# Optimization experiments

Measured on AMD Instinct MI355X. Metric: run time of the kernel, lower is better.

## Reference

```python
import jax, jax.numpy as jnp
import numpy as np

B, L, N = 32, 512, 512          # batch, seq_len, enc_in (num variables = token dim)
D, H, EL, DF = 512, 8, 2, 2048  # d_model, n_heads (hardcoded 8 in FourierBlock), e_layers, d_ff
PRED, K, MODES = 96, 25, 64     # pred_len, moving_avg kernel, fourier modes (low select)
E = D // H


def setup_inputs() -> dict:
    key = jax.random.key(0)
    ks = jax.random.split(key, 16)
    s = 0.02
    return {
        "x_enc": jax.random.normal(ks[0], (B, L, N), jnp.float32),
        "x_mark_enc": jax.random.normal(ks[1], (B, L, 4), jnp.float32),
        "x_dec": jax.random.normal(ks[2], (B, 144, N), jnp.float32),
        "x_mark_dec": jax.random.normal(ks[3], (B, 144, 4), jnp.float32),
        "W_trend": jax.random.normal(ks[4], (L, PRED), jnp.float32) * s,
        "b_trend": jnp.zeros((PRED,), jnp.float32),
        "W_emb": jax.random.normal(ks[5], (L, D), jnp.float32) * s,
        "b_emb": jnp.zeros((D,), jnp.float32),
        "Wq": jax.random.normal(ks[6], (EL, D, D), jnp.float32) * s,
        "bq": jnp.zeros((EL, D), jnp.float32),
        "Wk": jax.random.normal(ks[7], (EL, D, D), jnp.float32) * s,
        "bk": jnp.zeros((EL, D), jnp.float32),
        "Wv": jax.random.normal(ks[8], (EL, D, D), jnp.float32) * s,
        "bv": jnp.zeros((EL, D), jnp.float32),
        "fw_r": jax.random.uniform(ks[9], (EL, H, E, E, MODES), jnp.float32) / (D * D),
        "fw_i": jax.random.uniform(ks[10], (EL, H, E, E, MODES), jnp.float32) / (D * D),
        "Wo": jax.random.normal(ks[11], (EL, D, D), jnp.float32) * s,
        "bo": jnp.zeros((EL, D), jnp.float32),
        "W1": jax.random.normal(ks[12], (EL, DF, D), jnp.float32) * s,
        "W2": jax.random.normal(ks[13], (EL, D, DF), jnp.float32) * s,
        "ln_g": jnp.ones((D,), jnp.float32),
        "ln_b": jnp.zeros((D,), jnp.float32),
        "W_head": jax.random.normal(ks[14], (D, PRED), jnp.float32) * s,
        "b_head": jnp.zeros((PRED,), jnp.float32),
    }


def series_decomp(x, k):
    # moving average over axis=1 with edge replication padding (Autoformer style)
    pad = (k - 1) // 2
    xp = jnp.concatenate([jnp.repeat(x[:, :1], pad, axis=1), x,
                          jnp.repeat(x[:, -1:], pad, axis=1)], axis=1)
    c = jnp.cumsum(xp, axis=1)
    c = jnp.concatenate([jnp.zeros_like(c[:, :1]), c], axis=1)
    mean = (c[:, k:] - c[:, :-k]) / k
    return x - mean, mean


def fourier_attn(x, Wq, bq, Wk, bk, Wv, bv, fw, Wo, bo):
    # AutoCorrelationLayer wrapping FourierBlock (k/v projections computed but unused)
    b, n, d = x.shape
    q = (x @ Wq + bq).reshape(b, n, H, E)
    _k = (x @ Wk + bk).reshape(b, n, H, E)
    _v = (x @ Wv + bv).reshape(b, n, H, E)
    xq = jnp.transpose(q, (0, 2, 3, 1))        # [B,H,E,N]
    x_ft = jnp.fft.rfft(xq, axis=-1)           # [B,H,E,N//2+1]
    m = fw.shape[-1]
    # low-frequency mode select: index = range(m); out_ft[..., wi] = einsum('bhi,hio->bho')
    out_sel = jnp.einsum('bhim,hiom->bhom', x_ft[..., :m], fw)
    out_ft = jnp.zeros((b, H, E, n // 2 + 1), x_ft.dtype).at[..., :m].set(out_sel)
    xt = jnp.fft.irfft(out_ft, n=n, axis=-1)   # [B,H,E,N]
    out = xt.reshape(b, n, H * E)              # replicates torch .view(B, L, -1) on [B,H,E,L]
    return out @ Wo + bo


def encoder_layer(x, Wq, bq, Wk, bk, Wv, bv, fw, Wo, bo, W1, W2):
    x = x + fourier_attn(x, Wq, bq, Wk, bk, Wv, bv, fw, Wo, bo)
    x, _ = series_decomp(x, K)
    y = jax.nn.gelu(x @ W1.T, approximate=False) @ W2.T  # 1x1 convs, bias=False
    x, _ = series_decomp(x + y, K)
    return x


def my_layernorm(x, g, b):
    mu = jnp.mean(x, -1, keepdims=True)
    var = jnp.var(x, -1, keepdims=True)
    xh = (x - mu) / jnp.sqrt(var + 1e-5) * g + b
    return xh - jnp.mean(xh, axis=1, keepdims=True)  # my_Layernorm: subtract seq-mean


def reference(x_enc, x_mark_enc, x_dec, x_mark_dec, W_trend, b_trend, W_emb, b_emb,
              Wq, bq, Wk, bk, Wv, bv, fw_r, fw_i, Wo, bo, W1, W2, ln_g, ln_b,
              W_head, b_head):
    seasonal, trend = series_decomp(x_enc, K)                         # [B,L,N]
    trend_out = jnp.einsum('bln,lp->bpn', trend, W_trend) + b_trend[None, :, None]
    enc = jnp.einsum('bln,ld->bnd', seasonal, W_emb) + b_emb          # variate tokens [B,N,D]
    for i in range(EL):
        fw = fw_r[i] + 1j * fw_i[i]
        enc = encoder_layer(enc, Wq[i], bq[i], Wk[i], bk[i], Wv[i], bv[i],
                            fw, Wo[i], bo[i], W1[i], W2[i])
    enc = my_layernorm(enc, ln_g, ln_b)
    seasonal_out = jnp.transpose(enc @ W_head + b_head, (0, 2, 1))    # [B,pred,N]
    return seasonal_out + trend_out
```

## Files before the change

### kernel.cpp

```cpp
#include <hip/hip_runtime.h>
#include <math.h>


typedef unsigned short ushort_t;
typedef unsigned int uint_t;
using bf16x8_t = __attribute__((ext_vector_type(8))) short;
using f32x4_t  = __attribute__((ext_vector_type(4))) float;
using u16x8_t  = __attribute__((ext_vector_type(8))) unsigned short;

__device__ __forceinline__ unsigned short f2b(float x) {
    union { float f; uint_t u; } c; c.f = x;
    uint_t r = c.u + 0x7fffu + ((c.u >> 16) & 1u);
    return (unsigned short)(r >> 16);
}
__device__ __forceinline__ float b2f(unsigned short h) {
    union { uint_t u; float f; } c; c.u = ((uint_t)h) << 16; return c.f;
}
__device__ __forceinline__ float gelu_fast(float x) {
    float z = x * (1.5957691216f + 0.0713548163f * x * x);
    return x / (1.f + __expf(-z));
}

#define GCAST(p) ((const __attribute__((address_space(1))) void*)(p))
#define LCAST(p) ((__attribute__((address_space(3))) void*)(p))

enum { ME_F32 = 0, ME_BF16, ME_DCBIAS_BF16, ME_BIASCOL_BF16,
       ME_BIASCOL_ACCB16, ME_GELU_BF16, ME_RESB_BF16, ME_TREND };

template<int EPI>
__global__ __launch_bounds__(512)
void mgemm_k(const ushort_t* __restrict__ A, const ushort_t* __restrict__ B,
             const float* __restrict__ bias, const ushort_t* __restrict__ Resb,
             void* __restrict__ Cv,
             int M, int N, int K, int ldc, int ldres,
             long sA, long sB, long sC, long sRes)
{
    const int gx = gridDim.x, gy = gridDim.y;
    const int nwg = gx * gy * gridDim.z;
    const int lin = (blockIdx.z * gy + blockIdx.y) * gx + blockIdx.x;
    const int cpx = nwg >> 3;
    const int swz = (nwg & 7) ? lin : ((lin & 7) * cpx + (lin >> 3));
    const int bx = swz % gx;
    const int t2 = swz / gx;
    const int by = t2 % gy;
    const int bz = t2 / gy;

    A += bz * sA;
    B += bz * sB;
    const int m0 = by * 128, n0 = bx * 128;

    __shared__ __align__(16) ushort_t As[3][4096];
    __shared__ __align__(16) ushort_t Bs[3][4096];

    const int tid = threadIdx.x;
    const int wave = tid >> 6, lane = tid & 63;
    const int wr = wave >> 1, wc = wave & 1;

    f32x4_t acc[2][4] = {};

    const int srow = tid >> 2;
    const int skof = (((tid & 3) ^ ((tid >> 2) & 3)) << 3);

    const ushort_t* ga = A + (long)(m0 + srow) * K + skof;
    const ushort_t* gb = B + (long)(n0 + srow) * K + skof;
    const int nt = K >> 5;

#define STG(s, bidx) { const long ko = (long)(s) << 5; \
    __builtin_amdgcn_global_load_lds(GCAST(ga + ko), LCAST(As[bidx] + wave * 512), 16, 0, 0); \
    __builtin_amdgcn_global_load_lds(GCAST(gb + ko), LCAST(Bs[bidx] + wave * 512), 16, 0, 0); }

    STG(0, 0)
    STG(1, 1)

    const int q = lane >> 4;
    int cbuf = 0;

    for (int t = 0; t < nt; ++t) {
        if (t + 1 < nt) { asm volatile("s_waitcnt vmcnt(2)" ::: "memory"); }
        else            { asm volatile("s_waitcnt vmcnt(0)" ::: "memory"); }
        __builtin_amdgcn_s_barrier();
        asm volatile("" ::: "memory");
        __builtin_amdgcn_sched_barrier(0);
        if (t + 2 < nt) { int nb = cbuf + 2; if (nb >= 3) nb -= 3; STG(t + 2, nb) }

        bf16x8_t a[2], b[4];
        #pragma unroll
        for (int i = 0; i < 2; ++i) {
            int ra = wr * 32 + i * 16 + (lane & 15);
            a[i] = *(const bf16x8_t*)&As[cbuf][ra * 32 + ((q ^ (ra & 3)) << 3)];
        }
        #pragma unroll
        for (int j = 0; j < 4; ++j) {
            int rb = wc * 64 + j * 16 + (lane & 15);
            b[j] = *(const bf16x8_t*)&Bs[cbuf][rb * 32 + ((q ^ (rb & 3)) << 3)];
        }
        #pragma unroll
        for (int i = 0; i < 2; ++i)
            #pragma unroll
            for (int j = 0; j < 4; ++j)
                acc[i][j] = __builtin_amdgcn_mfma_f32_16x16x32_bf16(a[i], b[j], acc[i][j], 0, 0, 0);
        ++cbuf; if (cbuf >= 3) cbuf = 0;
    }
#undef STG

    float*    Cf  = (float*)Cv + bz * sC;
    ushort_t* Cb  = (ushort_t*)Cv + bz * sC;
    const ushort_t* R = Resb ? Resb + bz * sRes : nullptr;

    #pragma unroll
    for (int i = 0; i < 2; ++i) {
        #pragma unroll
        for (int j = 0; j < 4; ++j) {
            #pragma unroll
            for (int r = 0; r < 4; ++r) {
                int gm = m0 + wr * 32 + i * 16 + (lane >> 4) * 4 + r;
                int gn = n0 + wc * 64 + j * 16 + (lane & 15);
                float v = acc[i][j][r];
                long idx = (long)gm * ldc + gn;
                if (EPI == ME_F32)               Cf[idx] = v;
                else if (EPI == ME_BF16)         Cb[idx] = f2b(v);
                else if (EPI == ME_BIASCOL_BF16) Cb[idx] = f2b(v + bias[gn]);
                else if (EPI == ME_BIASCOL_ACCB16) Cb[idx] = f2b(b2f(Cb[idx]) + v + bias[gn]);
                else if (EPI == ME_GELU_BF16)    Cb[idx] = f2b(gelu_fast(v));
                else if (EPI == ME_RESB_BF16)    Cb[idx] = f2b(v + b2f(R[(long)gm * ldres + gn]));
            }
        }
    }
}

template<int EPI>
__global__ __launch_bounds__(256)
void sgemm_k(const ushort_t* __restrict__ A, const ushort_t* __restrict__ B,
             const float* __restrict__ bias, void* __restrict__ Cv,
             int M, int N, int K, int ldc,
             long sA, long sB, long sC)
{
    const int gx = gridDim.x, gy = gridDim.y;
    const int nwg = gx * gy * gridDim.z;
    const int lin = (blockIdx.z * gy + blockIdx.y) * gx + blockIdx.x;
    const int cpx = nwg >> 3;
    const int swz = (nwg & 7) ? lin : ((lin & 7) * cpx + (lin >> 3));
    const int bx = swz % gx;
    const int t2 = swz / gx;
    const int by = t2 % gy;
    const int bz = t2 / gy;

    A += bz * sA;
    B += bz * sB;
    const int m0 = by * 64, n0 = bx * 64;

    __shared__ __align__(16) ushort_t As[3][2048];
    __shared__ __align__(16) ushort_t Bs[3][2048];

    const int tid = threadIdx.x;
    const int wave = tid >> 6, lane = tid & 63;
    const int wr = wave >> 1, wc = wave & 1;

    f32x4_t acc[2][2] = {};

    const int srow = tid >> 2;
    const int skof = (((tid & 3) ^ ((tid >> 2) & 3)) << 3);

    const ushort_t* ga = A + (long)(m0 + srow) * K + skof;
    const ushort_t* gb = B + (long)(n0 + srow) * K + skof;
    const int nt = K >> 5;

#define STG(s, bidx) { const long ko = (long)(s) << 5; \
    __builtin_amdgcn_global_load_lds(GCAST(ga + ko), LCAST(As[bidx] + wave * 512), 16, 0, 0); \
    __builtin_amdgcn_global_load_lds(GCAST(gb + ko), LCAST(Bs[bidx] + wave * 512), 16, 0, 0); }

    STG(0, 0)
    STG(1, 1)

    const int q = lane >> 4;
    int cbuf = 0;

    for (int t = 0; t < nt; ++t) {
        if (t + 1 < nt) { asm volatile("s_waitcnt vmcnt(2)" ::: "memory"); }
        else            { asm volatile("s_waitcnt vmcnt(0)" ::: "memory"); }
        __builtin_amdgcn_s_barrier();
        asm volatile("" ::: "memory");
        __builtin_amdgcn_sched_barrier(0);
        if (t + 2 < nt) { int nb = cbuf + 2; if (nb >= 3) nb -= 3; STG(t + 2, nb) }

        bf16x8_t a[2], b[2];
        #pragma unroll
        for (int i = 0; i < 2; ++i) {
            int ra = wr * 32 + i * 16 + (lane & 15);
            a[i] = *(const bf16x8_t*)&As[cbuf][ra * 32 + ((q ^ (ra & 3)) << 3)];
        }
        #pragma unroll
        for (int j = 0; j < 2; ++j) {
            int rb = wc * 32 + j * 16 + (lane & 15);
            b[j] = *(const bf16x8_t*)&Bs[cbuf][rb * 32 + ((q ^ (rb & 3)) << 3)];
        }
        #pragma unroll
        for (int i = 0; i < 2; ++i)
            #pragma unroll
            for (int j = 0; j < 2; ++j)
                acc[i][j] = __builtin_amdgcn_mfma_f32_16x16x32_bf16(a[i], b[j], acc[i][j], 0, 0, 0);
        ++cbuf; if (cbuf >= 3) cbuf = 0;
    }
#undef STG

    float*    Cf = (float*)Cv + bz * sC;
    ushort_t* Cb = (ushort_t*)Cv + bz * sC;

    #pragma unroll
    for (int i = 0; i < 2; ++i) {
        #pragma unroll
        for (int j = 0; j < 2; ++j) {
            #pragma unroll
            for (int r = 0; r < 4; ++r) {
                int gm = m0 + wr * 32 + i * 16 + (lane >> 4) * 4 + r;
                int gn = n0 + wc * 32 + j * 16 + (lane & 15);
                float v = acc[i][j][r];
                long idx = (long)gm * ldc + gn;
                if (EPI == ME_F32)               Cf[idx] = v;
                else if (EPI == ME_BF16)         Cb[idx] = f2b(v);
                else if (EPI == ME_DCBIAS_BF16)  Cb[idx] = f2b(v + (gn == 0 ? 512.f * bias[gm] : 0.f));
                else if (EPI == ME_TREND) { if (gm < 96) Cf[idx] = v + bias[gm]; }
            }
        }
    }
}

__global__ __launch_bounds__(256)
void fmix_k(const ushort_t* __restrict__ A2, const ushort_t* __restrict__ B2,
            ushort_t* __restrict__ OS)
{
    const int hm = blockIdx.x;
    const int h = hm >> 6, m = hm & 63;
    __shared__ __align__(16) ushort_t As[32 * 128];
    __shared__ __align__(16) ushort_t Bs[128 * 128];

    const int tid = threadIdx.x;
    const int w = tid >> 6, lane = tid & 63;

    const ushort_t* Ag = A2 + (long)hm * 4096;
    const ushort_t* Bg = B2 + (long)hm * 16384;
    #pragma unroll
    for (int r = 0; r < 2; ++r) {
        int rowA = w * 8 + r * 4 + (lane >> 4);
        const ushort_t* src = Ag + rowA * 128 + (((lane & 15) ^ (rowA & 15)) << 3);
        __builtin_amdgcn_global_load_lds(GCAST(src), LCAST(As + w * 1024 + r * 512), 16, 0, 0);
    }
    #pragma unroll
    for (int r = 0; r < 8; ++r) {
        int rowB = w * 32 + r * 4 + (lane >> 4);
        const ushort_t* src = Bg + rowB * 128 + (((lane & 15) ^ (rowB & 15)) << 3);
        __builtin_amdgcn_global_load_lds(GCAST(src), LCAST(Bs + w * 4096 + r * 512), 16, 0, 0);
    }
    __syncthreads();

    f32x4_t acc[2][2] = {};
    #pragma unroll
    for (int kk = 0; kk < 4; ++kk) {
        const int cq = kk * 4 + (lane >> 4);
        bf16x8_t a[2], b[2];
        #pragma unroll
        for (int i = 0; i < 2; ++i) {
            int ra = i * 16 + (lane & 15);
            a[i] = *(const bf16x8_t*)&As[ra * 128 + ((cq ^ (ra & 15)) << 3)];
        }
        #pragma unroll
        for (int j = 0; j < 2; ++j) {
            int rb = w * 32 + j * 16 + (lane & 15);
            b[j] = *(const bf16x8_t*)&Bs[rb * 128 + ((cq ^ (rb & 15)) << 3)];
        }
        #pragma unroll
        for (int i = 0; i < 2; ++i)
            #pragma unroll
            for (int j = 0; j < 2; ++j)
                acc[i][j] = __builtin_amdgcn_mfma_f32_16x16x32_bf16(a[i], b[j], acc[i][j], 0, 0, 0);
    }

    #pragma unroll
    for (int i = 0; i < 2; ++i) {
        #pragma unroll
        for (int j = 0; j < 2; ++j) {
            #pragma unroll
            for (int r = 0; r < 4; ++r) {
                int b = i * 16 + (lane >> 4) * 4 + r;
                int n2 = w * 32 + j * 16 + (lane & 15);
                int o = n2 & 63, ri = n2 >> 6;
                OS[((long)b * 512 + h * 64 + o) * 128 + ri * 64 + m] = f2b(acc[i][j][r]);
            }
        }
    }
}

__global__ __launch_bounds__(256)
void bprep_k(const float* __restrict__ FR, const float* __restrict__ FI,
             ushort_t* __restrict__ B2)
{
    const int bx = blockIdx.x;
    const int h = bx >> 6, o = bx & 63;
    __shared__ float fr_s[64][65];
    __shared__ float fi_s[64][65];
    for (int e = threadIdx.x; e < 4096; e += 256) {
        int i = e >> 6, m = e & 63;
        long src = ((long)(h * 64 + i) * 64 + o) * 64 + m;
        fr_s[i][m] = FR[src];
        fi_s[i][m] = FI[src];
    }
    __syncthreads();
    const int m = threadIdx.x & 63;
    const int kq = threadIdx.x >> 6;
    ushort_t* b0 = B2 + ((long)(h * 64 + m) * 128 + o) * 128;
    ushort_t* b1 = B2 + ((long)(h * 64 + m) * 128 + o + 64) * 128;
    for (int kk = 0; kk < 32; ++kk) {
        int k2 = kq * 32 + kk;
        int ik = k2 & 63, hi = k2 >> 6;
        float fr = fr_s[ik][m], fi = fi_s[ik][m];
        b0[k2] = f2b(hi ? -fi : fr);
        b1[k2] = f2b(hi ?  fr : fi);
    }
}

__global__ __launch_bounds__(256)
void aprep_k(const ushort_t* __restrict__ XFTb, ushort_t* __restrict__ A2)
{
    const int bx = blockIdx.x;
    const int b = bx >> 3, h = bx & 7;
    __shared__ ushort_t xs[64][130];
    for (int e = threadIdx.x; e < 8192; e += 256) {
        int i = e >> 7, mp = e & 127;
        xs[i][mp] = XFTb[((long)b * 512 + h * 64 + i) * 128 + mp];
    }
    __syncthreads();
    const int m = threadIdx.x & 63;
    const int kq = threadIdx.x >> 6;
    ushort_t* dst = A2 + ((long)(h * 64 + m) * 32 + b) * 128;
    for (int kk = 0; kk < 32; ++kk) {
        int k2 = kq * 32 + kk;
        int i = k2 & 63, ri = k2 >> 6;
        dst[k2] = xs[i][ri * 64 + m];
    }
}

__global__ __launch_bounds__(256)
void decomp2t_k(const float* __restrict__ X, ushort_t* __restrict__ SbT,
                ushort_t* __restrict__ TrbT)
{
    const int id = blockIdx.x;
    const int ch = id & 1, rc = (id >> 1) & 31, b = id >> 6;
    const int c = ch * 256 + threadIdx.x;
    const int r0 = rc * 16;
    const long base = ((long)b << 18) + c;
    float s = 0.f;
    #pragma unroll
    for (int j = -12; j <= 12; ++j) {
        int rr = r0 + j; rr = rr < 0 ? 0 : (rr > 511 ? 511 : rr);
        s += X[base + ((long)rr << 9)];
    }
    u16x8_t sv0, sv1, tv0, tv1;
    for (int rr = 0; rr < 16; ++rr) {
        int r = r0 + rr;
        float mean = s * (1.f / 25.f);
        float x = X[base + ((long)r << 9)];
        if (rr < 8) { sv0[rr] = f2b(x - mean); tv0[rr] = f2b(mean); }
        else        { sv1[rr - 8] = f2b(x - mean); tv1[rr - 8] = f2b(mean); }
        int rp = r + 13; rp = rp > 511 ? 511 : rp;
        int rm = r - 12; rm = rm < 0 ? 0 : rm;
        s += X[base + ((long)rp << 9)] - X[base + ((long)rm << 9)];
    }
    long obase = (long)b * 262144 + (long)c * 512 + r0;
    *(u16x8_t*)&SbT[obase] = sv0;  *(u16x8_t*)&SbT[obase + 8] = sv1;
    *(u16x8_t*)&TrbT[obase] = tv0; *(u16x8_t*)&TrbT[obase + 8] = tv1;
}

__global__ __launch_bounds__(256)
void decomp2v_k(const ushort_t* __restrict__ Xb, ushort_t* __restrict__ Sb)
{
    const int id = blockIdx.x;
    const int b = id >> 4, rc = id & 15;
    const int c0 = (threadIdx.x & 63) * 8;
    const int rsub = threadIdx.x >> 6;
    const int r0 = rc * 32 + rsub * 8;
    const ushort_t* base = Xb + ((long)b << 18) + c0;
    ushort_t* obase = Sb + ((long)b << 18) + c0;

    float s[8] = {};
    #pragma unroll
    for (int j = -12; j <= 12; ++j) {
        int rr = r0 + j; rr = rr < 0 ? 0 : (rr > 511 ? 511 : rr);
        u16x8_t v = *(const u16x8_t*)(base + ((long)rr << 9));
        #pragma unroll
        for (int k = 0; k < 8; ++k) s[k] += b2f(v[k]);
    }
    for (int rr = 0; rr < 8; ++rr) {
        int r = r0 + rr;
        u16x8_t xv = *(const u16x8_t*)(base + ((long)r << 9));
        u16x8_t ov;
        #pragma unroll
        for (int k = 0; k < 8; ++k) ov[k] = f2b(b2f(xv[k]) - s[k] * (1.f / 25.f));
        *(u16x8_t*)(obase + ((long)r << 9)) = ov;
        int rp = r + 13; rp = rp > 511 ? 511 : rp;
        int rm = r - 12; rm = rm < 0 ? 0 : rm;
        u16x8_t vp = *(const u16x8_t*)(base + ((long)rp << 9));
        u16x8_t vm = *(const u16x8_t*)(base + ((long)rm << 9));
        #pragma unroll
        for (int k = 0; k < 8; ++k) s[k] += b2f(vp[k]) - b2f(vm[k]);
    }
}

__global__ __launch_bounds__(256)
void init_tables_k(ushort_t* __restrict__ TFb, ushort_t* __restrict__ TI2b)
{
    int t = blockIdx.x * 256 + threadIdx.x;
    const float w = 6.283185307179586f / 512.f;
    if (t < 65536) {
        int mp = t >> 9, n = t & 511;
        int m = mp & 63;
        float ang = ((m * n) & 511) * w;
        TFb[t] = f2b((mp < 64) ? cosf(ang) : -sinf(ang));
    } else {
        int u = t - 65536;
        int mp = u >> 9, n = u & 511;
        int m = mp & 63;
        float ang = ((m * n) & 511) * w;
        float v;
        if (mp < 64) v = (m == 0) ? (1.f / 512.f) : (2.f / 512.f) * cosf(ang);
        else         v = (m == 0) ? 0.f : -(2.f / 512.f) * sinf(ang);
        TI2b[u] = f2b(v);
    }
}

__global__ __launch_bounds__(256)
void f2b_k(const float* __restrict__ X, ushort_t* __restrict__ Y, long n)
{
    long i = ((long)blockIdx.x * 256 + threadIdx.x) * 8;
    if (i >= n) return;
    const float4* xp = (const float4*)(X + i);
    float4 v0 = xp[0], v1 = xp[1];
    u16x8_t o;
    o[0] = f2b(v0.x); o[1] = f2b(v0.y); o[2] = f2b(v0.z); o[3] = f2b(v0.w);
    o[4] = f2b(v1.x); o[5] = f2b(v1.y); o[6] = f2b(v1.z); o[7] = f2b(v1.w);
    *(u16x8_t*)(Y + i) = o;
}

__global__ __launch_bounds__(256)
void trans_b_k(const float* __restrict__ X, ushort_t* __restrict__ Y,
               int R, int C, long sX, long sY)
{
    __shared__ float t[32][33];
    X += (long)blockIdx.z * sX;
    Y += (long)blockIdx.z * sY;
    int r0 = blockIdx.y * 32, c0 = blockIdx.x * 32;
    int tx = threadIdx.x & 31, ty = threadIdx.x >> 5;
    #pragma unroll
    for (int i = ty; i < 32; i += 8)
        t[i][tx] = X[(long)(r0 + i) * C + c0 + tx];
    __syncthreads();
    #pragma unroll
    for (int i = ty; i < 32; i += 8)
        Y[(long)(c0 + i) * R + r0 + tx] = f2b(t[tx][i]);
}

__global__ __launch_bounds__(256)
void trans_bb_k(const ushort_t* __restrict__ X, ushort_t* __restrict__ Y,
                int R, int C, long sX, long sY)
{
    __shared__ ushort_t t[32][34];
    X += (long)blockIdx.z * sX;
    Y += (long)blockIdx.z * sY;
    int r0 = blockIdx.y * 32, c0 = blockIdx.x * 32;
    int tx = threadIdx.x & 31, ty = threadIdx.x >> 5;
    #pragma unroll
    for (int i = ty; i < 32; i += 8)
        t[i][tx] = X[(long)(r0 + i) * C + c0 + tx];
    __syncthreads();
    #pragma unroll
    for (int i = ty; i < 32; i += 8)
        Y[(long)(c0 + i) * R + r0 + tx] = t[tx][i];
}

__global__ __launch_bounds__(256)
void ln_rows_bb_k(const ushort_t* __restrict__ Xb, const float* __restrict__ g,
                  const float* __restrict__ bta, ushort_t* __restrict__ Yb)
{
    int wave = threadIdx.x >> 6, lane = threadIdx.x & 63;
    long row = (long)blockIdx.x * 4 + wave;
    const ushort_t* x = Xb + row * 512 + lane * 8;
    u16x8_t v = *(const u16x8_t*)x;
    float f[8];
    float s = 0.f, ss = 0.f;
    #pragma unroll
    for (int j = 0; j < 8; ++j) { f[j] = b2f(v[j]); s += f[j]; ss += f[j] * f[j]; }
    #pragma unroll
    for (int o = 32; o; o >>= 1) { s += __shfl_xor(s, o); ss += __shfl_xor(ss, o); }
    float mu = s * (1.f / 512.f);
    float var = ss * (1.f / 512.f) - mu * mu;
    float inv = rsqrtf(var + 1e-5f);
    u16x8_t ov;
    #pragma unroll
    for (int j = 0; j < 8; ++j)
        ov[j] = f2b((f[j] - mu) * inv * g[lane * 8 + j] + bta[lane * 8 + j]);
    *(u16x8_t*)(Yb + row * 512 + lane * 8) = ov;
}

__global__ __launch_bounds__(256)
void colmean_bb_k(const ushort_t* __restrict__ Y, ushort_t* __restrict__ O)
{
    __shared__ float ps[4][64];
    int b = blockIdx.x, dg = blockIdx.y;
    int wave = threadIdx.x >> 6, lane = threadIdx.x & 63;
    int d = dg * 64 + lane;
    long base = (long)b * 262144 + d;
    float s = 0.f;
    for (int t = wave * 128; t < wave * 128 + 128; ++t)
        s += b2f(Y[base + ((long)t << 9)]);
    ps[wave][lane] = s;
    __syncthreads();
    float mean = (ps[0][lane] + ps[1][lane] + ps[2][lane] + ps[3][lane]) * (1.f / 512.f);
    for (int t = wave * 128; t < wave * 128 + 128; ++t)
        O[base + ((long)t << 9)] = f2b(b2f(Y[base + ((long)t << 9)]) - mean);
}

__global__ __launch_bounds__(256)
void headadd_k(const float* __restrict__ Th, const float* __restrict__ bh,
               float* __restrict__ out)
{
    const int id = blockIdx.x;
    const int b = id >> 4, t0 = (id & 15) * 32;
    __shared__ float tile[32][100];
    for (int e = threadIdx.x; e < 32 * 96; e += 256) {
        int tl = e / 96, p = e - tl * 96;
        tile[tl][p] = Th[((long)(b * 512 + t0 + tl)) * 128 + p];
    }
    __syncthreads();
    for (int e = threadIdx.x; e < 96 * 32; e += 256) {
        int p = e >> 5, tl = e & 31;
        out[(long)b * 49152 + p * 512 + t0 + tl] += tile[tl][p] + bh[p];
    }
}

extern "C" void kernel_launch(void* const* d_in, const int* in_sizes, int n_in,
                              void* d_out, int out_size, void* d_ws, size_t ws_size,
                              hipStream_t stream)
{
    const float* x_enc   = (const float*)d_in[0];
    const float* W_trend = (const float*)d_in[4];
    const float* b_trend = (const float*)d_in[5];
    const float* W_emb   = (const float*)d_in[6];
    const float* b_emb   = (const float*)d_in[7];
    const float* Wq      = (const float*)d_in[8];
    const float* bq      = (const float*)d_in[9];
    const float* fw_r    = (const float*)d_in[14];
    const float* fw_i    = (const float*)d_in[15];
    const float* Wo      = (const float*)d_in[16];
    const float* bo      = (const float*)d_in[17];
    const float* W1      = (const float*)d_in[18];
    const float* W2      = (const float*)d_in[19];
    const float* ln_g    = (const float*)d_in[20];
    const float* ln_b    = (const float*)d_in[21];
    const float* W_head  = (const float*)d_in[22];
    const float* b_head  = (const float*)d_in[23];
    float* out = (float*)d_out;
    float* ws  = (float*)d_ws;

    const long F = 8388608;
    float* G    = ws;
    ushort_t* xw  = (ushort_t*)(ws + 3 * F);
    ushort_t* xs  = (ushort_t*)(ws + 4 * F);
    ushort_t* T1b = xs + 8388608;
    ushort_t* qT  = (ushort_t*)(ws + 5 * F);

    ushort_t* trendT = (ushort_t*)G;
    ushort_t* XFTb  = (ushort_t*)G;
    ushort_t* Yb    = (ushort_t*)(G + 1048576);
    ushort_t* A2    = (ushort_t*)(G + 2097152);
    ushort_t* OSELb = (ushort_t*)(G + 3145728);
    ushort_t* xbT   = (ushort_t*)(G + 4194304);
    ushort_t* B2    = (ushort_t*)(G + 8388608);
    float*    Thead = G;
    ushort_t* gb    = (ushort_t*)G;

    ushort_t* WembT  = (ushort_t*)(ws + 6 * F);
    ushort_t* WTq2   = WembT + 262144;
    ushort_t* WTo2   = WTq2 + 524288;
    ushort_t* W1b2   = WTo2 + 524288;
    ushort_t* W2b2   = W1b2 + 2097152;
    ushort_t* TFb    = W2b2 + 2097152;
    ushort_t* TI2b   = TFb + 65536;
    ushort_t* WtT    = TI2b + 65536;
    ushort_t* WheadT = WtT + 65536;
    ushort_t* TIWob2 = WheadT + 65536;

    dim3 blk(256), blk5(512);

    init_tables_k<<<dim3(512), blk, 0, stream>>>(TFb, TI2b);

    decomp2t_k<<<dim3(2048), blk, 0, stream>>>(x_enc, qT, trendT);

    trans_b_k<<<dim3(3, 16, 1), blk, 0, stream>>>(W_trend, WtT, 512, 96, 0L, 0L);
    trans_b_k<<<dim3(3, 16, 1), blk, 0, stream>>>(W_head, WheadT, 512, 96, 0L, 0L);
    trans_b_k<<<dim3(16, 16, 1), blk, 0, stream>>>(W_emb, WembT, 512, 512, 0L, 0L);
    trans_b_k<<<dim3(16, 16, 2), blk, 0, stream>>>(Wq, WTq2, 512, 512, 262144L, 262144L);
    trans_b_k<<<dim3(16, 16, 2), blk, 0, stream>>>(Wo, WTo2, 512, 512, 262144L, 262144L);
    f2b_k<<<dim3(1024), blk, 0, stream>>>(W1, W1b2, 2097152L);
    f2b_k<<<dim3(1024), blk, 0, stream>>>(W2, W2b2, 2097152L);
    sgemm_k<ME_BF16><<<dim3(2, 8, 2), blk, 0, stream>>>(
        WTo2, TI2b, nullptr, TIWob2,
        512, 128, 512, 128, 262144L, 0L, 65536L);

    sgemm_k<ME_TREND><<<dim3(8, 2, 32), blk, 0, stream>>>(
        WtT, trendT, b_trend, out,
        128, 512, 512, 512, 0L, 262144L, 49152L);

    mgemm_k<ME_BIASCOL_BF16><<<dim3(4, 4, 32), blk5, 0, stream>>>(
        qT, WembT, b_emb, nullptr, xw,
        512, 512, 512, 512, 0, 262144L, 0L, 262144L, 0L);

    for (int l = 0; l < 2; ++l) {
        const float* bq_l = bq + (long)l * 512;
        const float* bo_l = bo + (long)l * 512;
        const float* fr_l = fw_r + (long)l * 2097152;
        const float* fi_l = fw_i + (long)l * 2097152;
        const ushort_t* WTq_l   = WTq2 + (long)l * 262144;
        const ushort_t* W1b_l   = W1b2 + (long)l * 1048576;
        const ushort_t* W2b_l   = W2b2 + (long)l * 1048576;
        const ushort_t* TIWob_l = TIWob2 + (long)l * 65536;

        bprep_k<<<dim3(512), blk, 0, stream>>>(fr_l, fi_l, B2);

        trans_bb_k<<<dim3(16, 16, 32), blk, 0, stream>>>(xw, xbT, 512, 512, 262144L, 262144L);

        sgemm_k<ME_BF16><<<dim3(8, 2, 32), blk, 0, stream>>>(
            TFb, xbT, nullptr, Yb,
            128, 512, 512, 512, 0L, 262144L, 65536L);

        sgemm_k<ME_DCBIAS_BF16><<<dim3(2, 8, 32), blk, 0, stream>>>(
            WTq_l, Yb, bq_l, XFTb,
            512, 128, 512, 128, 0L, 65536L, 65536L);

        aprep_k<<<dim3(256), blk, 0, stream>>>(XFTb, A2);
        fmix_k<<<dim3(512), blk, 0, stream>>>(A2, B2, OSELb);

        mgemm_k<ME_BIASCOL_ACCB16><<<dim3(4, 128, 1), blk5, 0, stream>>>(
            OSELb, TIWob_l, bo_l, nullptr, xw,
            16384, 512, 128, 512, 0, 0L, 0L, 0L, 0L);

        decomp2v_k<<<dim3(512), blk, 0, stream>>>(xw, xs);

        mgemm_k<ME_GELU_BF16><<<dim3(16, 128, 1), blk5, 0, stream>>>(
            xs, W1b_l, nullptr, nullptr, gb,
            16384, 2048, 512, 2048, 0, 0L, 0L, 0L, 0L);
        mgemm_k<ME_RESB_BF16><<<dim3(4, 128, 1), blk5, 0, stream>>>(
            gb, W2b_l, nullptr, xs, T1b,
            16384, 512, 2048, 512, 512, 0L, 0L, 0L, 0L);

        decomp2v_k<<<dim3(512), blk, 0, stream>>>(T1b, xw);
    }

    ln_rows_bb_k<<<dim3(4096), blk, 0, stream>>>(xw, ln_g, ln_b, T1b);
    colmean_bb_k<<<dim3(32, 8), blk, 0, stream>>>(T1b, xs);

    sgemm_k<ME_F32><<<dim3(2, 256, 1), blk, 0, stream>>>(
        xs, WheadT, nullptr, Thead,
        16384, 128, 512, 128, 0L, 0L, 0L);

    headadd_k<<<dim3(512), blk, 0, stream>>>(Thead, b_head, out);
}
```

Before: 546.1 us.

## Halve mgemm block to four waves with larger per-wave tiles, drop LDS swizzle

The 128x128 mgemm now runs with 256 threads instead of 512. Each wave computes a 64x64 sub-tile (4x4 MFMA accumulators) instead of 32x64, and each thread issues two global-to-LDS loads per operand per stage. The XOR swizzle on the LDS layout is removed in favour of a plain row-major 32-wide layout. The aim is more MFMA work per LDS fragment load and fewer waves to synchronise, at the cost of more accumulator registers, lower occupancy, and likely LDS bank conflicts on the fragment reads.

```diff
diff --git a/kernel.cpp b/kernel.cpp
--- a/kernel.cpp
+++ b/kernel.cpp
@@ -28,7 +28,7 @@
        ME_BIASCOL_ACCB16, ME_GELU_BF16, ME_RESB_BF16, ME_TREND };
 
 template<int EPI>
-__global__ __launch_bounds__(512)
+__global__ __launch_bounds__(256)
 void mgemm_k(const ushort_t* __restrict__ A, const ushort_t* __restrict__ B,
              const float* __restrict__ bias, const ushort_t* __restrict__ Resb,
              void* __restrict__ Cv,
@@ -56,46 +56,42 @@
     const int wave = tid >> 6, lane = tid & 63;
     const int wr = wave >> 1, wc = wave & 1;
 
-    f32x4_t acc[2][4] = {};
-
-    const int srow = tid >> 2;
-    const int skof = (((tid & 3) ^ ((tid >> 2) & 3)) << 3);
-
-    const ushort_t* ga = A + (long)(m0 + srow) * K + skof;
-    const ushort_t* gb = B + (long)(n0 + srow) * K + skof;
+    f32x4_t acc[4][4] = {};
+
+    const ushort_t* ga = A + (long)(m0 + wave * 32 + (lane >> 2)) * K + (lane & 3) * 8;
+    const ushort_t* gb = B + (long)(n0 + wave * 32 + (lane >> 2)) * K + (lane & 3) * 8;
+    const long row16 = (long)16 * K;
     const int nt = K >> 5;
 
 #define STG(s, bidx) { const long ko = (long)(s) << 5; \
-    __builtin_amdgcn_global_load_lds(GCAST(ga + ko), LCAST(As[bidx] + wave * 512), 16, 0, 0); \
-    __builtin_amdgcn_global_load_lds(GCAST(gb + ko), LCAST(Bs[bidx] + wave * 512), 16, 0, 0); }
+    __builtin_amdgcn_global_load_lds(GCAST(ga + ko),         LCAST(As[bidx] + wave * 1024),       16, 0, 0); \
+    __builtin_amdgcn_global_load_lds(GCAST(ga + ko + row16), LCAST(As[bidx] + wave * 1024 + 512), 16, 0, 0); \
+    __builtin_amdgcn_global_load_lds(GCAST(gb + ko),         LCAST(Bs[bidx] + wave * 1024),       16, 0, 0); \
+    __builtin_amdgcn_global_load_lds(GCAST(gb + ko + row16), LCAST(Bs[bidx] + wave * 1024 + 512), 16, 0, 0); }
 
     STG(0, 0)
     STG(1, 1)
 
-    const int q = lane >> 4;
+    const int kg = (lane >> 4) * 8;
     int cbuf = 0;
 
     for (int t = 0; t < nt; ++t) {
-        if (t + 1 < nt) { asm volatile("s_waitcnt vmcnt(2)" ::: "memory"); }
+        if (t + 1 < nt) { asm volatile("s_waitcnt vmcnt(4)" ::: "memory"); }
         else            { asm volatile("s_waitcnt vmcnt(0)" ::: "memory"); }
         __builtin_amdgcn_s_barrier();
         asm volatile("" ::: "memory");
         __builtin_amdgcn_sched_barrier(0);
         if (t + 2 < nt) { int nb = cbuf + 2; if (nb >= 3) nb -= 3; STG(t + 2, nb) }
 
-        bf16x8_t a[2], b[4];
-        #pragma unroll
-        for (int i = 0; i < 2; ++i) {
-            int ra = wr * 32 + i * 16 + (lane & 15);
-            a[i] = *(const bf16x8_t*)&As[cbuf][ra * 32 + ((q ^ (ra & 3)) << 3)];
-        }
-        #pragma unroll
-        for (int j = 0; j < 4; ++j) {
-            int rb = wc * 64 + j * 16 + (lane & 15);
-            b[j] = *(const bf16x8_t*)&Bs[cbuf][rb * 32 + ((q ^ (rb & 3)) << 3)];
-        }
-        #pragma unroll
-        for (int i = 0; i < 2; ++i)
+        bf16x8_t a[4], b[4];
+        #pragma unroll
+        for (int i = 0; i < 4; ++i)
+            a[i] = *(const bf16x8_t*)&As[cbuf][(wr * 64 + i * 16 + (lane & 15)) * 32 + kg];
+        #pragma unroll
+        for (int j = 0; j < 4; ++j)
+            b[j] = *(const bf16x8_t*)&Bs[cbuf][(wc * 64 + j * 16 + (lane & 15)) * 32 + kg];
+        #pragma unroll
+        for (int i = 0; i < 4; ++i)
             #pragma unroll
             for (int j = 0; j < 4; ++j)
                 acc[i][j] = __builtin_amdgcn_mfma_f32_16x16x32_bf16(a[i], b[j], acc[i][j], 0, 0, 0);
@@ -108,12 +104,12 @@
     const ushort_t* R = Resb ? Resb + bz * sRes : nullptr;
 
     #pragma unroll
-    for (int i = 0; i < 2; ++i) {
+    for (int i = 0; i < 4; ++i) {
         #pragma unroll
         for (int j = 0; j < 4; ++j) {
             #pragma unroll
             for (int r = 0; r < 4; ++r) {
-                int gm = m0 + wr * 32 + i * 16 + (lane >> 4) * 4 + r;
+                int gm = m0 + wr * 64 + i * 16 + (lane >> 4) * 4 + r;
                 int gn = n0 + wc * 64 + j * 16 + (lane & 15);
                 float v = acc[i][j][r];
                 long idx = (long)gm * ldc + gn;
@@ -158,8 +154,8 @@
 
     f32x4_t acc[2][2] = {};
 
+    const int skof = (((tid & 3) ^ ((tid >> 2) & 3)) << 3);
     const int srow = tid >> 2;
-    const int skof = (((tid & 3) ^ ((tid >> 2) & 3)) << 3);
 
     const ushort_t* ga = A + (long)(m0 + srow) * K + skof;
     const ushort_t* gb = B + (long)(n0 + srow) * K + skof;
@@ -588,7 +584,7 @@
     ushort_t* WheadT = WtT + 65536;
     ushort_t* TIWob2 = WheadT + 65536;
 
-    dim3 blk(256), blk5(512);
+    dim3 blk(256);
 
     init_tables_k<<<dim3(512), blk, 0, stream>>>(TFb, TI2b);
 
@@ -609,7 +605,7 @@
         WtT, trendT, b_trend, out,
         128, 512, 512, 512, 0L, 262144L, 49152L);
 
-    mgemm_k<ME_BIASCOL_BF16><<<dim3(4, 4, 32), blk5, 0, stream>>>(
+    mgemm_k<ME_BIASCOL_BF16><<<dim3(4, 4, 32), blk, 0, stream>>>(
         qT, WembT, b_emb, nullptr, xw,
         512, 512, 512, 512, 0, 262144L, 0L, 262144L, 0L);
 
@@ -638,16 +634,16 @@
         aprep_k<<<dim3(256), blk, 0, stream>>>(XFTb, A2);
         fmix_k<<<dim3(512), blk, 0, stream>>>(A2, B2, OSELb);
 
-        mgemm_k<ME_BIASCOL_ACCB16><<<dim3(4, 128, 1), blk5, 0, stream>>>(
+        mgemm_k<ME_BIASCOL_ACCB16><<<dim3(4, 128, 1), blk, 0, stream>>>(
             OSELb, TIWob_l, bo_l, nullptr, xw,
             16384, 512, 128, 512, 0, 0L, 0L, 0L, 0L);
 
         decomp2v_k<<<dim3(512), blk, 0, stream>>>(xw, xs);
 
-        mgemm_k<ME_GELU_BF16><<<dim3(16, 128, 1), blk5, 0, stream>>>(
+        mgemm_k<ME_GELU_BF16><<<dim3(16, 128, 1), blk, 0, stream>>>(
             xs, W1b_l, nullptr, nullptr, gb,
             16384, 2048, 512, 2048, 0, 0L, 0L, 0L, 0L);
-        mgemm_k<ME_RESB_BF16><<<dim3(4, 128, 1), blk5, 0, stream>>>(
+        mgemm_k<ME_RESB_BF16><<<dim3(4, 128, 1), blk, 0, stream>>>(
             gb, W2b_l, nullptr, xs, T1b,
             16384, 512, 2048, 512, 512, 0L, 0L, 0L, 0L);
 
```

After: 557.5 us. 2.1% more time.
